# Performance work log

Hardware: AMD Instinct MI355X
Metric: run time of the kernel (lower is better)

The kernel has to match this reference:

```python
import jax, jax.numpy as jnp
import numpy as np

NUM_LABELS = [5, 9, 13, 17, 21, 25, 29, 33, 37, 41, 45, 49, 53, 57, 61, 65]
N_TASKS = len(NUM_LABELS)
LMAX = max(NUM_LABELS) - 1  # 64, max number of thresholds per task
B = 1048576


def setup_inputs() -> dict:
    key = jax.random.key(0)
    k1, k2, k3 = jax.random.split(key, 3)
    inp = jax.random.normal(k1, (B, 1), dtype=jnp.float32)
    task_ids = jax.random.randint(k2, (B,), 0, N_TASKS, dtype=jnp.int32)
    lengths = jnp.array([nl - 1 for nl in NUM_LABELS], dtype=jnp.int32)  # [n_tasks]
    # offsets: normal init, sorted ascending (as in reset_parameters); dense padded table
    offsets = jnp.sort(jax.random.normal(k3, (N_TASKS, LMAX), dtype=jnp.float32), axis=-1)
    # 'multi' discrimination, non-exp init -> ones
    discrimination = jnp.ones((N_TASKS, LMAX), dtype=jnp.float32)
    return {
        "input": inp,
        "task_ids": task_ids,
        "offsets": offsets,
        "discrimination": discrimination,
        "lengths": lengths,
    }


def reference(input, task_ids, offsets, discrimination, lengths):
    # Ragged gather + elementwise affine, padded to LMAX and masked.
    # out[i, k] = disc[task_ids[i], k] * (input[i, 0] + off[task_ids[i], k])  for k < lengths[task_ids[i]]
    valid = jnp.arange(LMAX, dtype=jnp.int32)[None, :] < lengths[task_ids][:, None]  # [B, LMAX]
    out = discrimination[task_ids] * (input[:, :1] + offsets[task_ids])
    return jnp.where(valid, out, jnp.zeros((), dtype=out.dtype))
```

## Files before the change

### kernel.cpp

```cpp
#include <hip/hip_runtime.h>

#define N_TASKS 16
#define LMAX 64

typedef float f32x4 __attribute__((ext_vector_type(4)));

__global__ __launch_bounds__(256) void MultiElementWiseAffine_kernel(
    const float* __restrict__ input,
    const int*   __restrict__ task_ids,
    const float* __restrict__ offsets,
    const float* __restrict__ disc,
    const int*   __restrict__ lengths,
    f32x4*       __restrict__ out,
    int total4)
{
    __shared__ alignas(16) float s_tab[N_TASKS * 2 * LMAX];

    for (int i = threadIdx.x; i < N_TASKS * LMAX; i += blockDim.x) {
        int t = i >> 6;
        int k = i & (LMAX - 1);
        float m = (k < lengths[t]) ? disc[i] : 0.0f;
        s_tab[t * 128 + k]      = m;
        s_tab[t * 128 + 64 + k] = m * offsets[i];
    }
    __syncthreads();

    const int stride = gridDim.x * blockDim.x;
    int g = blockIdx.x * blockDim.x + threadIdx.x;
    if (g >= total4) return;

    int   t_cur = task_ids[g >> 4];
    float x_cur = input[g >> 4];

    for (; g < total4; g += stride) {
        int gn      = g + stride;
        int rown    = (gn < total4 ? gn : g) >> 4;
        int t_nxt   = task_ids[rown];
        float x_nxt = input[rown];

        int k4 = g & 15;
        const float* base = &s_tab[t_cur * 128 + (k4 << 2)];
        f32x4 mv = *(const f32x4*)(base);
        f32x4 pv = *(const f32x4*)(base + 64);
        f32x4 r;
        r.x = fmaf(mv.x, x_cur, pv.x);
        r.y = fmaf(mv.y, x_cur, pv.y);
        r.z = fmaf(mv.z, x_cur, pv.z);
        r.w = fmaf(mv.w, x_cur, pv.w);
        __builtin_nontemporal_store(r, &out[g]);

        t_cur = t_nxt;
        x_cur = x_nxt;
    }
}

extern "C" void kernel_launch(void* const* d_in, const int* in_sizes, int n_in,
                              void* d_out, int out_size, void* d_ws, size_t ws_size,
                              hipStream_t stream) {
    const float* input    = (const float*)d_in[0];
    const int*   task_ids = (const int*)d_in[1];
    const float* offsets  = (const float*)d_in[2];
    const float* disc     = (const float*)d_in[3];
    const int*   lengths  = (const int*)d_in[4];
    f32x4*       out      = (f32x4*)d_out;

    int total4 = out_size / 4;
    int block  = 256;
    int grid   = 2048;

    MultiElementWiseAffine_kernel<<<grid, block, 0, stream>>>(
        input, task_ids, offsets, disc, lengths, out, total4);
}
```

Measured before the change: 52.60 us.

## Stage per-row inputs in shared memory and assign fixed row chunks per block

Each block now handles a contiguous chunk of 512 rows. It first loads those rows' input values and task ids into shared memory with coalesced loads, then runs a fully unrolled loop of 32 iterations that reads them from LDS. This replaces the grid-stride loop, where every thread redundantly loaded task_id and input from global memory, with software prefetch of the next row. The grid grows to total4/8192 blocks, so each block reloads the table setup (B/512 = 2048 blocks, the same count as before) and adds a sync before the stores.

New measurement: 56.15 us. 6.8% more time.

```diff
diff --git a/kernel.cpp b/kernel.cpp
--- a/kernel.cpp
+++ b/kernel.cpp
@@ -2,8 +2,12 @@
 
 #define N_TASKS 16
 #define LMAX 64
+#define ROWS_PER_BLOCK 512
+#define F4_PER_BLOCK (ROWS_PER_BLOCK * 16)
+#define ITERS (F4_PER_BLOCK / 256)
 
 typedef float f32x4 __attribute__((ext_vector_type(4)));
+typedef float f32x2 __attribute__((ext_vector_type(2)));
 
 __global__ __launch_bounds__(256) void MultiElementWiseAffine_kernel(
     const float* __restrict__ input,
@@ -14,43 +18,65 @@
     f32x4*       __restrict__ out,
     int total4)
 {
-    __shared__ alignas(16) float s_tab[N_TASKS * 2 * LMAX];
+    __shared__ alignas(16) float s_tab[N_TASKS * 128];
+    __shared__ alignas(8) f32x2 s_row[ROWS_PER_BLOCK];
 
-    for (int i = threadIdx.x; i < N_TASKS * LMAX; i += blockDim.x) {
-        int t = i >> 6;
-        int k = i & (LMAX - 1);
+    const int tid    = threadIdx.x;
+    const int n_rows = total4 >> 4;
+    const int row0   = blockIdx.x * ROWS_PER_BLOCK;
+
+    for (int i = tid; i < N_TASKS * LMAX; i += 256) {
+        int t = i >> 6, k = i & (LMAX - 1);
         float m = (k < lengths[t]) ? disc[i] : 0.0f;
         s_tab[t * 128 + k]      = m;
         s_tab[t * 128 + 64 + k] = m * offsets[i];
     }
+    for (int i = tid; i < ROWS_PER_BLOCK; i += 256) {
+        int r = row0 + i;
+        f32x2 v;
+        v.x = (r < n_rows) ? input[r] : 0.0f;
+        v.y = __int_as_float((r < n_rows) ? task_ids[r] : 0);
+        s_row[i] = v;
+    }
     __syncthreads();
 
-    const int stride = gridDim.x * blockDim.x;
-    int g = blockIdx.x * blockDim.x + threadIdx.x;
-    if (g >= total4) return;
+    const int  k4    = tid & 15;
+    const int  lr0   = tid >> 4;
+    const long gbase = (long)blockIdx.x * F4_PER_BLOCK + tid;
 
-    int   t_cur = task_ids[g >> 4];
-    float x_cur = input[g >> 4];
-
-    for (; g < total4; g += stride) {
-        int gn      = g + stride;
-        int rown    = (gn < total4 ? gn : g) >> 4;
-        int t_nxt   = task_ids[rown];
-        float x_nxt = input[rown];
-
-        int k4 = g & 15;
-        const float* base = &s_tab[t_cur * 128 + (k4 << 2)];
-        f32x4 mv = *(const f32x4*)(base);
-        f32x4 pv = *(const f32x4*)(base + 64);
-        f32x4 r;
-        r.x = fmaf(mv.x, x_cur, pv.x);
-        r.y = fmaf(mv.y, x_cur, pv.y);
-        r.z = fmaf(mv.z, x_cur, pv.z);
-        r.w = fmaf(mv.w, x_cur, pv.w);
-        __builtin_nontemporal_store(r, &out[g]);
-
-        t_cur = t_nxt;
-        x_cur = x_nxt;
+    if (gbase + (ITERS - 1) * 256 < total4) {
+        #pragma unroll
+        for (int it = 0; it < ITERS; ++it) {
+            f32x2 rv = s_row[lr0 + it * 16];
+            float x  = rv.x;
+            int   t  = __float_as_int(rv.y);
+            const float* base = &s_tab[t * 128 + (k4 << 2)];
+            f32x4 mv = *(const f32x4*)(base);
+            f32x4 pv = *(const f32x4*)(base + 64);
+            f32x4 r;
+            r.x = fmaf(mv.x, x, pv.x);
+            r.y = fmaf(mv.y, x, pv.y);
+            r.z = fmaf(mv.z, x, pv.z);
+            r.w = fmaf(mv.w, x, pv.w);
+            __builtin_nontemporal_store(r, &out[gbase + it * 256]);
+        }
+    } else {
+        for (int it = 0; it < ITERS; ++it) {
+            long g = gbase + it * 256;
+            if (g >= total4) break;
+            f32x2 rv = s_row[lr0 + it * 16];
+            float x  = rv.x;
+            int   t  = __float_as_int(rv.y);
+            const float* base = &s_tab[t * 128 + (k4 << 2)];
+            f32x4 mv = *(const f32x4*)(base);
+            f32x4 pv = *(const f32x4*)(base + 64);
+            f32x4 r;
+            r.x = fmaf(mv.x, x, pv.x);
+            r.y = fmaf(mv.y, x, pv.y);
+            r.z = fmaf(mv.z, x, pv.z);
+            r.w = fmaf(mv.w, x, pv.w);
+            __builtin_nontemporal_store(r, &out[g]);
+        }
     }
 }
 
@@ -65,9 +91,8 @@
     f32x4*       out      = (f32x4*)d_out;
 
     int total4 = out_size / 4;
-    int block  = 256;
-    int grid   = 2048;
+    int grid   = (total4 + F4_PER_BLOCK - 1) / F4_PER_BLOCK;
 
-    MultiElementWiseAffine_kernel<<<grid, block, 0, stream>>>(
+    MultiElementWiseAffine_kernel<<<grid, 256, 0, stream>>>(
         input, task_ids, offsets, disc, lengths, out, total4);
 }
```
